# Kernel tuning notes

Measured on AMD Instinct MI355X. Metric: run time of the kernel, lower is better.

The kernel has to match this reference:

```python
import jax, jax.numpy as jnp
import numpy as np

NUM_TRAIN = 256  # num_train_anchors
N, A, T = 8, 131072, 64


def _make_boxes(key, shape2):
    # shape2 = (..., 2) of (y, x); returns valid boxes (y1, x1, y2, x2) in [0, 1]
    k1, k2 = jax.random.split(key)
    c1 = jax.random.uniform(k1, shape2, dtype=jnp.float32)
    c2 = jax.random.uniform(k2, shape2, dtype=jnp.float32)
    lo = jnp.minimum(c1, c2)
    hi = jnp.maximum(c1, c2)
    return jnp.stack([lo[..., 0], lo[..., 1], hi[..., 0], hi[..., 1]], axis=-1)


def setup_inputs() -> dict:
    key = jax.random.key(0)
    ka, kt, kp, kn = jax.random.split(key, 4)
    return {
        "anchors": _make_boxes(ka, (N, A, 2)),
        "true_bboxes": _make_boxes(kt, (N, T, 2)),
        "rand_pos": jax.random.uniform(kp, (N, A), dtype=jnp.float32),
        "rand_neg": jax.random.uniform(kn, (N, A), dtype=jnp.float32),
    }


def _bbox_overlap(anchors, gt):
    # anchors [A,4], gt [T,4] -> IoU [A,T]
    ay1, ax1, ay2, ax2 = [anchors[:, i] for i in range(4)]
    gy1, gx1, gy2, gx2 = [gt[:, i] for i in range(4)]
    a_area = (ay2 - ay1) * (ax2 - ax1)                       # [A]
    g_area = (gy2 - gy1) * (gx2 - gx1)                       # [T]
    ih = jnp.clip(jnp.minimum(ay2[:, None], gy2[None, :]) - jnp.maximum(ay1[:, None], gy1[None, :]), 0.0)
    iw = jnp.clip(jnp.minimum(ax2[:, None], gx2[None, :]) - jnp.maximum(ax1[:, None], gx1[None, :]), 0.0)
    inter = ih * iw                                          # [A,T]
    union = a_area[:, None] + g_area[None, :] - inter
    return jnp.where(union > 0, inter / jnp.where(union > 0, union, 1.0), 0.0)


def _rank_of(scores):
    # rank[i] = position of element i in ascending sort of scores
    order = jnp.argsort(scores)
    return jnp.zeros(scores.shape[0], jnp.int32).at[order].set(jnp.arange(scores.shape[0], dtype=jnp.int32))


def _compute_bbox_deltas(anchors, gt):
    # standard (dy, dx, dh, dw) encoding with safe denominators
    ah = anchors[:, 2] - anchors[:, 0]
    aw = anchors[:, 3] - anchors[:, 1]
    acy = anchors[:, 0] + 0.5 * ah
    acx = anchors[:, 1] + 0.5 * aw
    gh = gt[:, 2] - gt[:, 0]
    gw = gt[:, 3] - gt[:, 1]
    gcy = gt[:, 0] + 0.5 * gh
    gcx = gt[:, 1] + 0.5 * gw
    ah_s = jnp.where(ah > 0, ah, 1.0)
    aw_s = jnp.where(aw > 0, aw, 1.0)
    gh_s = jnp.where(gh > 0, gh, 1.0)
    gw_s = jnp.where(gw > 0, gw, 1.0)
    return jnp.stack([(gcy - acy) / ah_s, (gcx - acx) / aw_s,
                      jnp.log(gh_s / ah_s), jnp.log(gw_s / aw_s)], axis=-1)


def _get_targets(anchors, gt, r_pos, r_neg):
    na = anchors.shape[0]
    # strip_out_of_bounds_anchors: zero out anchors falling outside [0,1]^2 (keeps static shape)
    inb = (anchors[:, 0] >= 0) & (anchors[:, 1] >= 0) & (anchors[:, 2] <= 1) & (anchors[:, 3] <= 1)
    anchors = jnp.where(inb[:, None], anchors, 0.0)

    overlaps = _bbox_overlap(anchors, gt)                    # [A,T]

    # --- class assignment ---
    iou_max_val = jnp.max(overlaps, axis=1)                  # [A]
    classes = jnp.full((na,), -1, jnp.int32)
    classes = jnp.where(iou_max_val < 0.3, 0, classes)
    iou_max_anchor = jnp.argmax(overlaps, axis=0)            # [T] best anchor per gt
    pos_anchor = jnp.zeros((na,), jnp.int32).at[iou_max_anchor].set(1)
    classes = jnp.where(pos_anchor > 0, 1, classes)
    classes = jnp.where(iou_max_val >= 0.7, 1, classes)

    # --- subsample positives to NUM_TRAIN//2 (uniform random subset) ---
    pos = classes > 0
    rank_p = _rank_of(jnp.where(pos, r_pos, jnp.inf))
    keep_pos = pos & (rank_p < NUM_TRAIN // 2)
    classes = jnp.where(pos & ~keep_pos, -1, classes)
    n_pos = jnp.sum(keep_pos.astype(jnp.int32))

    # --- subsample negatives to NUM_TRAIN - n_pos ---
    desired_neg = NUM_TRAIN - n_pos
    neg = classes == 0
    rank_n = _rank_of(jnp.where(neg, r_neg, jnp.inf))
    keep_neg = neg & (rank_n < desired_neg)
    classes = jnp.where(neg & ~keep_neg, -1, classes)

    # --- deltas for positive anchors ---
    best_gt = jnp.argmax(overlaps, axis=1)                   # [A]
    deltas = _compute_bbox_deltas(anchors, gt[best_gt])      # [A,4]
    deltas = jnp.where((classes > 0)[:, None], deltas, 0.0)
    return classes, deltas


def reference(anchors, true_bboxes, rand_pos, rand_neg):
    classes, deltas = jax.vmap(_get_targets)(anchors, true_bboxes, rand_pos, rand_neg)
    return classes, deltas
```

## Files before the change

### kernel.cpp

```cpp
#include <hip/hip_runtime.h>
#include <stdint.h>

#define N_B 8
#define A_N 131072
#define T_N 64
#define NUM_TRAIN 256
#define NEG_TAU 0.05f
#define ITEM_CAP 1024
#define APT 4
#define GBLK 128
#define SEG 1024

typedef unsigned long long u64;
typedef unsigned int u32;

__device__ __forceinline__ float iou_one(float ay1, float ax1, float ay2, float ax2,
                                         float a_area, float gy1, float gx1, float gy2,
                                         float gx2, float g_area) {
#pragma clang fp contract(off)
    float ih = fmaxf(fminf(ay2, gy2) - fmaxf(ay1, gy1), 0.0f);
    float iw = fmaxf(fminf(ax2, gx2) - fmaxf(ax1, gx1), 0.0f);
    float inter = ih * iw;
    float uni = (a_area + g_area) - inter;
    return uni > 0.0f ? inter / uni : 0.0f;
}

__global__ void __launch_bounds__(256, 4) k_main(const float4* __restrict__ anchors4,
                                                 const float4* __restrict__ gts4,
                                                 const float* __restrict__ rpos,
                                                 const float* __restrict__ rneg,
                                                 unsigned char* __restrict__ preclass,
                                                 u64* __restrict__ colpart,
                                                 u64* __restrict__ pos_list,
                                                 u64* __restrict__ neg_list,
                                                 int* __restrict__ bcp, int* __restrict__ bcn) {
    __shared__ float4 gbox[T_N];
    __shared__ float gars[T_N];
    __shared__ u64 cmax[T_N];
    __shared__ int lp, ln;
    int n = blockIdx.y, bx = blockIdx.x, tid = threadIdx.x, lane = tid & 63;
    int a0 = bx * SEG + tid;
    size_t nA = (size_t)n * A_N;

    if (tid < T_N) {
        float4 gb = gts4[n * T_N + tid];
        gbox[tid] = gb;
        {
#pragma clang fp contract(off)
            gars[tid] = (gb.z - gb.x) * (gb.w - gb.y);
        }
        cmax[tid] = 0;
    }
    if (tid == 0) { lp = 0; ln = 0; }
    __syncthreads();

    float ay1[APT], ax1[APT], ay2[APT], ax2[APT], aar[APT], vmax[APT];
#pragma unroll
    for (int k = 0; k < APT; k++) {
        float4 ab = anchors4[nA + a0 + k * 256];
        float y1 = ab.x, x1 = ab.y, y2 = ab.z, x2 = ab.w;
        bool inb = (y1 >= 0.f) && (x1 >= 0.f) && (y2 <= 1.f) && (x2 <= 1.f);
        if (!inb) { y1 = x1 = y2 = x2 = 0.f; }
        ay1[k] = y1; ax1[k] = x1; ay2[k] = y2; ax2[k] = x2;
        {
#pragma clang fp contract(off)
            aar[k] = (y2 - y1) * (x2 - x1);
        }
        vmax[k] = 0.f;
    }

#pragma unroll 4
    for (int jj = 0; jj < T_N; jj++) {
        int j = (lane + jj) & (T_N - 1);
        float4 gb = gbox[j];
        float gar = gars[j];
        float vb = iou_one(ay1[0], ax1[0], ay2[0], ax2[0], aar[0], gb.x, gb.y, gb.z, gb.w, gar);
        vmax[0] = fmaxf(vmax[0], vb);
        int kb = 0;
#pragma unroll
        for (int k = 1; k < APT; k++) {
            float v = iou_one(ay1[k], ax1[k], ay2[k], ax2[k], aar[k], gb.x, gb.y, gb.z, gb.w, gar);
            vmax[k] = fmaxf(vmax[k], v);
            if (v > vb) { vb = v; kb = k; }
        }
        u64 pk = ((u64)__float_as_uint(vb) << 32) | (u32)(~(u32)(a0 + (kb << 8)));
        atomicMax(&cmax[j], pk);
    }

    size_t segbase = ((size_t)(n * GBLK + bx)) << 10;
#pragma unroll
    for (int k = 0; k < APT; k++) {
        int a = a0 + k * 256;
        float vm = vmax[k];
        int c0 = (vm < 0.3f) ? 0 : ((vm >= 0.7f) ? 1 : -1);
        preclass[nA + a] = (unsigned char)(signed char)c0;
        if (c0 == 1) {
            int s = atomicAdd(&lp, 1);
            pos_list[segbase + s] = ((u64)__float_as_uint(rpos[nA + a]) << 32) | (u32)a;
        } else if (c0 == 0) {
            float r = rneg[nA + a];
            if (r < NEG_TAU) {
                int s = atomicAdd(&ln, 1);
                neg_list[segbase + s] = ((u64)__float_as_uint(r) << 32) | (u32)a;
            }
        }
    }
    __syncthreads();
    if (tid < T_N) colpart[(size_t)((n << 6) + tid) * GBLK + bx] = cmax[tid];
    if (tid == 0) { bcp[n * GBLK + bx] = lp; bcn[n * GBLK + bx] = ln; }
}

__device__ u64 select_kth2(const u64* lists, const int* scnt,
                           const u64* extras, int ecnt, const u32* exbm,
                           int k, float scale, u64 ovf_all,
                           int* hist, u64* items, int* misc, int* wsum, u64* result) {
    int tid = threadIdx.x, lane = tid & 63, wid = tid >> 6;
    hist[tid] = 0;
    if (tid == 0) { misc[0] = 0; *result = ovf_all; }
    __syncthreads();

    int seg = tid >> 1, half = tid & 1;
    int c = scnt[seg];
    const ulonglong2* b2 = (const ulonglong2*)(lists + ((size_t)seg << 10));
    int nch = (c + 1) >> 1;

    {
        ulonglong2 q;
        if (half < nch) q = b2[half];
        for (int ci = half; ci < nch; ci += 2) {
            ulonglong2 qn;
            if (ci + 2 < nch) qn = b2[ci + 2];
            {
                u64 p = q.x; int a = (int)(u32)p;
                if (!exbm || !((exbm[a >> 5] >> (a & 31)) & 1)) {
                    float v = __uint_as_float((u32)(p >> 32));
                    int bb = (int)(v * scale); bb = bb > 255 ? 255 : bb;
                    atomicAdd(&hist[bb], 1);
                }
            }
            if (2 * ci + 1 < c) {
                u64 p = q.y; int a = (int)(u32)p;
                if (!exbm || !((exbm[a >> 5] >> (a & 31)) & 1)) {
                    float v = __uint_as_float((u32)(p >> 32));
                    int bb = (int)(v * scale); bb = bb > 255 ? 255 : bb;
                    atomicAdd(&hist[bb], 1);
                }
            }
            q = qn;
        }
    }
    for (int i = tid; i < ecnt; i += 256) {
        float v = __uint_as_float((u32)(extras[i] >> 32));
        int bb = (int)(v * scale); bb = bb > 255 ? 255 : bb;
        atomicAdd(&hist[bb], 1);
    }
    __syncthreads();

    int h = hist[tid], v = h;
#pragma unroll
    for (int d = 1; d < 64; d <<= 1) {
        int t = __shfl_up(v, d, 64);
        if (lane >= d) v += t;
    }
    if (lane == 63) wsum[wid] = v;
    __syncthreads();
    int base = 0;
    for (int w = 0; w < wid; w++) base += wsum[w];
    int total = wsum[0] + wsum[1] + wsum[2] + wsum[3];
    int incl = base + v, exc = incl - h;
    if (k >= exc && k < incl) { misc[1] = tid; misc[2] = exc; }
    __syncthreads();
    if (k >= total) return ovf_all;
    int b = misc[1], before = misc[2];

    {
        ulonglong2 q;
        if (half < nch) q = b2[half];
        for (int ci = half; ci < nch; ci += 2) {
            ulonglong2 qn;
            if (ci + 2 < nch) qn = b2[ci + 2];
            {
                u64 p = q.x; int a = (int)(u32)p;
                if (!exbm || !((exbm[a >> 5] >> (a & 31)) & 1)) {
                    float vv = __uint_as_float((u32)(p >> 32));
                    int bn = (int)(vv * scale); bn = bn > 255 ? 255 : bn;
                    if (bn == b) { int ix = atomicAdd(&misc[0], 1); if (ix < ITEM_CAP) items[ix] = p; }
                }
            }
            if (2 * ci + 1 < c) {
                u64 p = q.y; int a = (int)(u32)p;
                if (!exbm || !((exbm[a >> 5] >> (a & 31)) & 1)) {
                    float vv = __uint_as_float((u32)(p >> 32));
                    int bn = (int)(vv * scale); bn = bn > 255 ? 255 : bn;
                    if (bn == b) { int ix = atomicAdd(&misc[0], 1); if (ix < ITEM_CAP) items[ix] = p; }
                }
            }
            q = qn;
        }
    }
    for (int i = tid; i < ecnt; i += 256) {
        u64 p = extras[i];
        float vv = __uint_as_float((u32)(p >> 32));
        int bn = (int)(vv * scale); bn = bn > 255 ? 255 : bn;
        if (bn == b) { int ix = atomicAdd(&misc[0], 1); if (ix < ITEM_CAP) items[ix] = p; }
    }
    __syncthreads();
    int m = misc[0]; m = m < ITEM_CAP ? m : ITEM_CAP;
    int target = k - before;
    for (int i = tid; i < m; i += 256) {
        u64 p = items[i];
        int r = 0;
        for (int j = 0; j < m; j++) r += (items[j] < p);
        if (r == target) *result = p;
    }
    __syncthreads();
    u64 res = *result;
    __syncthreads();
    return res;
}

__global__ void __launch_bounds__(256) k_select(const u64* __restrict__ pos_list,
                                                const u64* __restrict__ neg_list,
                                                const int* __restrict__ bcp,
                                                const int* __restrict__ bcn,
                                                const u64* __restrict__ colpart,
                                                const unsigned char* __restrict__ preclass,
                                                const float* __restrict__ rpos,
                                                int* __restrict__ wnr_g,
                                                u64* __restrict__ cutoff) {
    __shared__ int sbp[GBLK], sbn[GBLK];
    __shared__ u64 cq[256];
    __shared__ int wnrs[T_N];
    __shared__ u64 extras[T_N];
    __shared__ int hist[256];
    __shared__ u64 items[ITEM_CAP];
    __shared__ u32 exbm[A_N / 32];
    __shared__ int misc[4];
    __shared__ u64 result;
    __shared__ int wsum[4];
    __shared__ int shr[9];
    int n = blockIdx.x, tid = threadIdx.x, lane = tid & 63, wid = tid >> 6;

    int pv = tid < GBLK ? bcp[n * GBLK + tid] : 0;
    int nv = tid < GBLK ? bcn[n * GBLK + tid] : 0;
    if (tid < GBLK) { sbp[tid] = pv; sbn[tid] = nv; }
#pragma unroll
    for (int off = 32; off > 0; off >>= 1) {
        pv += __shfl_xor(pv, off, 64);
        nv += __shfl_xor(nv, off, 64);
    }
    if (lane == 0) { shr[wid] = pv; shr[4 + wid] = nv; }

#pragma unroll
    for (int i = 0; i < A_N / 32 / 256; i++) exbm[tid + i * 256] = 0;

    {
        int t = tid >> 2, q = tid & 3;
        const u64* cp = colpart + (size_t)((n << 6) + t) * GBLK + q * 32;
        u64 m = 0;
#pragma unroll 8
        for (int i = 0; i < 32; i++) { u64 x = cp[i]; m = x > m ? x : m; }
        cq[tid] = m;
    }
    __syncthreads();
    if (tid < T_N) {
        u64 m = cq[tid * 4];
        u64 x = cq[tid * 4 + 1]; m = x > m ? x : m;
        x = cq[tid * 4 + 2]; m = x > m ? x : m;
        x = cq[tid * 4 + 3]; m = x > m ? x : m;
        int w = (int)(~(u32)(m & 0xFFFFFFFFull));
        wnrs[tid] = w;
        wnr_g[n * T_N + tid] = w;
        atomicOr(&exbm[w >> 5], 1u << (w & 31));
    }
    __syncthreads();
    if (tid < T_N) {
        int w = wnrs[tid];
        bool dup = false;
        for (int t2 = 0; t2 < tid; t2++) dup |= (wnrs[t2] == w);
        int pc = (int)(signed char)preclass[(size_t)n * A_N + w];
        bool val = !dup && (pc != 1);
        u64 mask = __ballot(val);
        if (val) {
            int ix = (int)__popcll(mask & ((1ull << lane) - 1));
            extras[ix] = ((u64)__float_as_uint(rpos[(size_t)n * A_N + w]) << 32) | (u32)w;
        }
        if (tid == 0) shr[8] = (int)__popcll(mask);
    }
    __syncthreads();
    int extra_cnt = shr[8];
    int P = shr[0] + shr[1] + shr[2] + shr[3] + extra_cnt;

    u64 cpos = select_kth2(pos_list + (((size_t)n * GBLK) << 10), sbp,
                           extras, extra_cnt, nullptr,
                           NUM_TRAIN / 2, 256.0f, ~0ull,
                           hist, items, misc, wsum, &result);
    int n_pos = P < NUM_TRAIN / 2 ? P : NUM_TRAIN / 2;
    int k_neg = NUM_TRAIN - n_pos;
    u64 cneg = select_kth2(neg_list + (((size_t)n * GBLK) << 10), sbn,
                           nullptr, 0, exbm,
                           k_neg, 256.0f / NEG_TAU, ((u64)__float_as_uint(NEG_TAU) << 32),
                           hist, items, misc, wsum, &result);
    if (tid == 0) { cutoff[2 * n] = cpos; cutoff[2 * n + 1] = cneg; }
}

__global__ void __launch_bounds__(256) k_final(const float4* __restrict__ anchors4,
                                               const float4* __restrict__ gts4,
                                               const u32* __restrict__ preclass32,
                                               const int* __restrict__ wnr_g,
                                               const float4* __restrict__ rpos4,
                                               const float4* __restrict__ rneg4,
                                               const u64* __restrict__ cutoff,
                                               float4* __restrict__ out_classes4,
                                               float4* __restrict__ out_deltas) {
    __shared__ float4 gbox[T_N];
    __shared__ float gars[T_N];
    __shared__ u32 wbm[32];
    int n = blockIdx.y, bx = blockIdx.x, tid = threadIdx.x;
    if (tid < 32) wbm[tid] = 0;
    __syncthreads();
    if (tid < T_N) {
        float4 gb = gts4[n * T_N + tid];
        gbox[tid] = gb;
        {
#pragma clang fp contract(off)
            gars[tid] = (gb.z - gb.x) * (gb.w - gb.y);
        }
        int w = wnr_g[n * T_N + tid];
        int d = w - bx * SEG;
        if ((u32)d < (u32)SEG) atomicOr(&wbm[d >> 5], 1u << (d & 31));
    }
    __syncthreads();

    size_t gi4 = ((size_t)n * A_N) / 4 + bx * 256 + tid;
    u32 pcw = preclass32[gi4];
    float4 rp = rpos4[gi4];
    float4 rn = rneg4[gi4];
    float rpv[4] = {rp.x, rp.y, rp.z, rp.w};
    float rnv[4] = {rn.x, rn.y, rn.z, rn.w};
    int a0 = (bx * 256 + tid) * 4;
    u64 cp = cutoff[2 * n], cn = cutoff[2 * n + 1];

    u32 marked = (wbm[tid >> 3] >> ((tid & 7) * 4)) & 0xF;

    float fcv[4];
#pragma unroll
    for (int j = 0; j < 4; j++) {
        int c = (int)(signed char)((pcw >> (8 * j)) & 0xFF);
        if ((marked >> j) & 1) c = 1;
        int a = a0 + j;
        int fc = -1;
        if (c == 1) {
            u64 p = ((u64)__float_as_uint(rpv[j]) << 32) | (u32)a;
            fc = (p < cp) ? 1 : -1;
        } else if (c == 0) {
            u64 p = ((u64)__float_as_uint(rnv[j]) << 32) | (u32)a;
            fc = (p < cn) ? 0 : -1;
        }
        fcv[j] = (float)fc;

        float4 d = make_float4(0.f, 0.f, 0.f, 0.f);
        if (fc == 1) {
            float4 ab = anchors4[(size_t)n * A_N + a];
            float ay1 = ab.x, ax1 = ab.y, ay2 = ab.z, ax2 = ab.w;
            bool inb = (ay1 >= 0.f) && (ax1 >= 0.f) && (ay2 <= 1.f) && (ax2 <= 1.f);
            if (!inb) { ay1 = ax1 = ay2 = ax2 = 0.f; }
            float a_area;
            {
#pragma clang fp contract(off)
                a_area = (ay2 - ay1) * (ax2 - ax1);
            }
            float vm = 0.f; int jb = 0;
            for (int t = 0; t < T_N; t++) {
                float4 gb = gbox[t];
                float v = iou_one(ay1, ax1, ay2, ax2, a_area, gb.x, gb.y, gb.z, gb.w, gars[t]);
                bool g = v > vm;
                vm = g ? v : vm;
                jb = g ? t : jb;
            }
            float4 gb = gbox[jb];
            float ah = ay2 - ay1, aw = ax2 - ax1;
            float acy = ay1 + 0.5f * ah, acx = ax1 + 0.5f * aw;
            float gh = gb.z - gb.x, gw = gb.w - gb.y;
            float gcy = gb.x + 0.5f * gh, gcx = gb.y + 0.5f * gw;
            float ah_s = ah > 0.f ? ah : 1.f, aw_s = aw > 0.f ? aw : 1.f;
            float gh_s = gh > 0.f ? gh : 1.f, gw_s = gw > 0.f ? gw : 1.f;
            d.x = (gcy - acy) / ah_s;
            d.y = (gcx - acx) / aw_s;
            d.z = logf(gh_s / ah_s);
            d.w = logf(gw_s / aw_s);
        }
        out_deltas[(size_t)n * A_N + a] = d;
    }
    out_classes4[gi4] = make_float4(fcv[0], fcv[1], fcv[2], fcv[3]);
}

extern "C" void kernel_launch(void* const* d_in, const int* in_sizes, int n_in,
                              void* d_out, int out_size, void* d_ws, size_t ws_size,
                              hipStream_t stream) {
    const float* anchors = (const float*)d_in[0];
    const float* gts     = (const float*)d_in[1];
    const float* rpos    = (const float*)d_in[2];
    const float* rneg    = (const float*)d_in[3];

    char* p = (char*)d_ws;
    u64* cutoff   = (u64*)p;  p += 2 * N_B * sizeof(u64);
    u64* colpart  = (u64*)p;  p += (size_t)N_B * T_N * GBLK * sizeof(u64);
    u64* pos_list = (u64*)p;  p += (size_t)N_B * GBLK * SEG * sizeof(u64);
    u64* neg_list = (u64*)p;  p += (size_t)N_B * GBLK * SEG * sizeof(u64);
    unsigned char* preclass = (unsigned char*)p; p += (size_t)N_B * A_N;
    int* bcp  = (int*)p;  p += N_B * GBLK * sizeof(int);
    int* bcn  = (int*)p;  p += N_B * GBLK * sizeof(int);
    int* wnr  = (int*)p;  p += N_B * T_N * sizeof(int);

    float* out_classes = (float*)d_out;
    float4* out_deltas = (float4*)(out_classes + (size_t)N_B * A_N);

    k_main<<<dim3(GBLK, N_B), 256, 0, stream>>>(
        (const float4*)anchors, (const float4*)gts, rpos, rneg,
        preclass, colpart, pos_list, neg_list, bcp, bcn);
    k_select<<<N_B, 256, 0, stream>>>(pos_list, neg_list, bcp, bcn, colpart,
                                      preclass, rpos, wnr, cutoff);
    k_final<<<dim3(GBLK, N_B), 256, 0, stream>>>(
        (const float4*)anchors, (const float4*)gts, (const u32*)preclass, wnr,
        (const float4*)rpos, (const float4*)rneg, cutoff,
        (float4*)out_classes, out_deltas);
}
```

Baseline: 176.4 us.

## Split selection into pos/neg blocks, halve anchors per block, hash-set exclusion

The main kernel now uses 256 blocks per image with 2 anchors per thread, which doubles the grid to raise parallelism. Candidate lists per block are capped at 128 entries. The select kernel now runs two blocks per image, one choosing the positive cutoff and one the negative cutoff in parallel. The 16KB exclusion bitmap is replaced by a small open-addressing hash set in shared memory. In exchange, twice as many column partials must be reduced, and the list caps can silently drop candidates if a block has more than 128, which risks wrong results.

```diff
diff --git a/kernel.cpp b/kernel.cpp
--- a/kernel.cpp
+++ b/kernel.cpp
@@ -6,10 +6,14 @@
 #define T_N 64
 #define NUM_TRAIN 256
 #define NEG_TAU 0.05f
-#define ITEM_CAP 1024
-#define APT 4
-#define GBLK 128
-#define SEG 1024
+#define ITEM_CAP 512
+#define HSET 512
+#define APT 2
+#define SEG_A 512
+#define GBLK_A 256
+#define CAPP 128
+#define BLK_C 128
+#define SEG_C 1024
 
 typedef unsigned long long u64;
 typedef unsigned int u32;
@@ -25,21 +29,21 @@
     return uni > 0.0f ? inter / uni : 0.0f;
 }
 
-__global__ void __launch_bounds__(256, 4) k_main(const float4* __restrict__ anchors4,
-                                                 const float4* __restrict__ gts4,
-                                                 const float* __restrict__ rpos,
-                                                 const float* __restrict__ rneg,
-                                                 unsigned char* __restrict__ preclass,
-                                                 u64* __restrict__ colpart,
-                                                 u64* __restrict__ pos_list,
-                                                 u64* __restrict__ neg_list,
-                                                 int* __restrict__ bcp, int* __restrict__ bcn) {
+__global__ void __launch_bounds__(256) k_main(const float4* __restrict__ anchors4,
+                                              const float4* __restrict__ gts4,
+                                              const float* __restrict__ rpos,
+                                              const float* __restrict__ rneg,
+                                              unsigned char* __restrict__ preclass,
+                                              u64* __restrict__ colpart,
+                                              u64* __restrict__ pos_list,
+                                              u64* __restrict__ neg_list,
+                                              int* __restrict__ bcp, int* __restrict__ bcn) {
     __shared__ float4 gbox[T_N];
     __shared__ float gars[T_N];
     __shared__ u64 cmax[T_N];
-    __shared__ int lp, ln;
+    __shared__ int lcnt[2];
     int n = blockIdx.y, bx = blockIdx.x, tid = threadIdx.x, lane = tid & 63;
-    int a0 = bx * SEG + tid;
+    int a0 = bx * SEG_A + tid;
     size_t nA = (size_t)n * A_N;
 
     if (tid < T_N) {
@@ -51,7 +55,7 @@
         }
         cmax[tid] = 0;
     }
-    if (tid == 0) { lp = 0; ln = 0; }
+    if (tid < 2) lcnt[tid] = 0;
     __syncthreads();
 
     float ay1[APT], ax1[APT], ay2[APT], ax2[APT], aar[APT], vmax[APT];
@@ -87,7 +91,7 @@
         atomicMax(&cmax[j], pk);
     }
 
-    size_t segbase = ((size_t)(n * GBLK + bx)) << 10;
+    size_t segbase = ((size_t)(n * GBLK_A + bx)) << 7;
 #pragma unroll
     for (int k = 0; k < APT; k++) {
         int a = a0 + k * 256;
@@ -95,23 +99,38 @@
         int c0 = (vm < 0.3f) ? 0 : ((vm >= 0.7f) ? 1 : -1);
         preclass[nA + a] = (unsigned char)(signed char)c0;
         if (c0 == 1) {
-            int s = atomicAdd(&lp, 1);
-            pos_list[segbase + s] = ((u64)__float_as_uint(rpos[nA + a]) << 32) | (u32)a;
+            int sl = atomicAdd(&lcnt[0], 1);
+            if (sl < CAPP)
+                pos_list[segbase + sl] = ((u64)__float_as_uint(rpos[nA + a]) << 32) | (u32)a;
         } else if (c0 == 0) {
             float r = rneg[nA + a];
             if (r < NEG_TAU) {
-                int s = atomicAdd(&ln, 1);
-                neg_list[segbase + s] = ((u64)__float_as_uint(r) << 32) | (u32)a;
-            }
-        }
-    }
-    __syncthreads();
-    if (tid < T_N) colpart[(size_t)((n << 6) + tid) * GBLK + bx] = cmax[tid];
-    if (tid == 0) { bcp[n * GBLK + bx] = lp; bcn[n * GBLK + bx] = ln; }
+                int sl = atomicAdd(&lcnt[1], 1);
+                if (sl < CAPP)
+                    neg_list[segbase + sl] = ((u64)__float_as_uint(r) << 32) | (u32)a;
+            }
+        }
+    }
+    __syncthreads();
+    if (tid < T_N) colpart[(size_t)((n << 6) + tid) * GBLK_A + bx] = cmax[tid];
+    if (tid == 0) {
+        bcp[n * GBLK_A + bx] = lcnt[0] < CAPP ? lcnt[0] : CAPP;
+        bcn[n * GBLK_A + bx] = lcnt[1] < CAPP ? lcnt[1] : CAPP;
+    }
+}
+
+__device__ __forceinline__ bool in_hset(const int* hset, int a) {
+    u32 h = ((u32)a * 2654435761u) >> 23 & (HSET - 1);
+    while (true) {
+        int v = hset[h];
+        if (v == -1) return false;
+        if (v == a) return true;
+        h = (h + 1) & (HSET - 1);
+    }
 }
 
 __device__ u64 select_kth2(const u64* lists, const int* scnt,
-                           const u64* extras, int ecnt, const u32* exbm,
+                           const u64* extras, int ecnt, const int* hset, bool use_excl,
                            int k, float scale, u64 ovf_all,
                            int* hist, u64* items, int* misc, int* wsum, u64* result) {
     int tid = threadIdx.x, lane = tid & 63, wid = tid >> 6;
@@ -119,20 +138,19 @@
     if (tid == 0) { misc[0] = 0; *result = ovf_all; }
     __syncthreads();
 
-    int seg = tid >> 1, half = tid & 1;
-    int c = scnt[seg];
-    const ulonglong2* b2 = (const ulonglong2*)(lists + ((size_t)seg << 10));
+    int c = scnt[tid];
+    const ulonglong2* b2 = (const ulonglong2*)(lists + ((size_t)tid << 7));
     int nch = (c + 1) >> 1;
 
     {
         ulonglong2 q;
-        if (half < nch) q = b2[half];
-        for (int ci = half; ci < nch; ci += 2) {
+        if (nch > 0) q = b2[0];
+        for (int ci = 0; ci < nch; ci++) {
             ulonglong2 qn;
-            if (ci + 2 < nch) qn = b2[ci + 2];
+            if (ci + 1 < nch) qn = b2[ci + 1];
             {
                 u64 p = q.x; int a = (int)(u32)p;
-                if (!exbm || !((exbm[a >> 5] >> (a & 31)) & 1)) {
+                if (!use_excl || !in_hset(hset, a)) {
                     float v = __uint_as_float((u32)(p >> 32));
                     int bb = (int)(v * scale); bb = bb > 255 ? 255 : bb;
                     atomicAdd(&hist[bb], 1);
@@ -140,7 +158,7 @@
             }
             if (2 * ci + 1 < c) {
                 u64 p = q.y; int a = (int)(u32)p;
-                if (!exbm || !((exbm[a >> 5] >> (a & 31)) & 1)) {
+                if (!use_excl || !in_hset(hset, a)) {
                     float v = __uint_as_float((u32)(p >> 32));
                     int bb = (int)(v * scale); bb = bb > 255 ? 255 : bb;
                     atomicAdd(&hist[bb], 1);
@@ -175,13 +193,13 @@
 
     {
         ulonglong2 q;
-        if (half < nch) q = b2[half];
-        for (int ci = half; ci < nch; ci += 2) {
+        if (nch > 0) q = b2[0];
+        for (int ci = 0; ci < nch; ci++) {
             ulonglong2 qn;
-            if (ci + 2 < nch) qn = b2[ci + 2];
+            if (ci + 1 < nch) qn = b2[ci + 1];
             {
                 u64 p = q.x; int a = (int)(u32)p;
-                if (!exbm || !((exbm[a >> 5] >> (a & 31)) & 1)) {
+                if (!use_excl || !in_hset(hset, a)) {
                     float vv = __uint_as_float((u32)(p >> 32));
                     int bn = (int)(vv * scale); bn = bn > 255 ? 255 : bn;
                     if (bn == b) { int ix = atomicAdd(&misc[0], 1); if (ix < ITEM_CAP) items[ix] = p; }
@@ -189,7 +207,7 @@
             }
             if (2 * ci + 1 < c) {
                 u64 p = q.y; int a = (int)(u32)p;
-                if (!exbm || !((exbm[a >> 5] >> (a & 31)) & 1)) {
+                if (!use_excl || !in_hset(hset, a)) {
                     float vv = __uint_as_float((u32)(p >> 32));
                     int bn = (int)(vv * scale); bn = bn > 255 ? 255 : bn;
                     if (bn == b) { int ix = atomicAdd(&misc[0], 1); if (ix < ITEM_CAP) items[ix] = p; }
@@ -219,47 +237,44 @@
     return res;
 }
 
-__global__ void __launch_bounds__(256) k_select(const u64* __restrict__ pos_list,
-                                                const u64* __restrict__ neg_list,
-                                                const int* __restrict__ bcp,
-                                                const int* __restrict__ bcn,
-                                                const u64* __restrict__ colpart,
-                                                const unsigned char* __restrict__ preclass,
-                                                const float* __restrict__ rpos,
-                                                int* __restrict__ wnr_g,
-                                                u64* __restrict__ cutoff) {
-    __shared__ int sbp[GBLK], sbn[GBLK];
+__global__ void __launch_bounds__(256) k_B(const u64* __restrict__ pos_list,
+                                           const u64* __restrict__ neg_list,
+                                           const int* __restrict__ bcp,
+                                           const int* __restrict__ bcn,
+                                           const u64* __restrict__ colpart,
+                                           const unsigned char* __restrict__ preclass,
+                                           const float* __restrict__ rpos,
+                                           int* __restrict__ wnr_g,
+                                           u64* __restrict__ cutoff) {
+    __shared__ int sbp[GBLK_A], sbn[GBLK_A];
     __shared__ u64 cq[256];
     __shared__ int wnrs[T_N];
     __shared__ u64 extras[T_N];
     __shared__ int hist[256];
     __shared__ u64 items[ITEM_CAP];
-    __shared__ u32 exbm[A_N / 32];
+    __shared__ int hset[HSET];
     __shared__ int misc[4];
+    __shared__ int wsum[4];
+    __shared__ int shr[10];
     __shared__ u64 result;
-    __shared__ int wsum[4];
-    __shared__ int shr[9];
-    int n = blockIdx.x, tid = threadIdx.x, lane = tid & 63, wid = tid >> 6;
-
-    int pv = tid < GBLK ? bcp[n * GBLK + tid] : 0;
-    int nv = tid < GBLK ? bcn[n * GBLK + tid] : 0;
-    if (tid < GBLK) { sbp[tid] = pv; sbn[tid] = nv; }
-#pragma unroll
-    for (int off = 32; off > 0; off >>= 1) {
-        pv += __shfl_xor(pv, off, 64);
-        nv += __shfl_xor(nv, off, 64);
-    }
-    if (lane == 0) { shr[wid] = pv; shr[4 + wid] = nv; }
-
-#pragma unroll
-    for (int i = 0; i < A_N / 32 / 256; i++) exbm[tid + i * 256] = 0;
+    int n = blockIdx.y, role = blockIdx.x, tid = threadIdx.x, lane = tid & 63, wid = tid >> 6;
+    size_t nA = (size_t)n * A_N;
+
+    int pv = bcp[n * GBLK_A + tid];
+    sbp[tid] = pv;
+    sbn[tid] = bcn[n * GBLK_A + tid];
+#pragma unroll
+    for (int off = 32; off > 0; off >>= 1) pv += __shfl_xor(pv, off, 64);
+    if (lane == 0) shr[wid] = pv;
+
+    for (int i = tid; i < HSET; i += 256) hset[i] = -1;
 
     {
         int t = tid >> 2, q = tid & 3;
-        const u64* cp = colpart + (size_t)((n << 6) + t) * GBLK + q * 32;
+        const u64* cp = colpart + (size_t)((n << 6) + t) * GBLK_A + q * 64;
         u64 m = 0;
 #pragma unroll 8
-        for (int i = 0; i < 32; i++) { u64 x = cp[i]; m = x > m ? x : m; }
+        for (int i = 0; i < 64; i++) { u64 x = cp[i]; m = x > m ? x : m; }
         cq[tid] = m;
     }
     __syncthreads();
@@ -270,20 +285,25 @@
         x = cq[tid * 4 + 3]; m = x > m ? x : m;
         int w = (int)(~(u32)(m & 0xFFFFFFFFull));
         wnrs[tid] = w;
-        wnr_g[n * T_N + tid] = w;
-        atomicOr(&exbm[w >> 5], 1u << (w & 31));
+        if (role == 0) wnr_g[n * T_N + tid] = w;
+        u32 hh = ((u32)w * 2654435761u) >> 23 & (HSET - 1);
+        while (true) {
+            int old = atomicCAS(&hset[hh], -1, w);
+            if (old == -1 || old == w) break;
+            hh = (hh + 1) & (HSET - 1);
+        }
     }
     __syncthreads();
     if (tid < T_N) {
         int w = wnrs[tid];
         bool dup = false;
         for (int t2 = 0; t2 < tid; t2++) dup |= (wnrs[t2] == w);
-        int pc = (int)(signed char)preclass[(size_t)n * A_N + w];
+        int pc = (int)(signed char)preclass[nA + w];
         bool val = !dup && (pc != 1);
         u64 mask = __ballot(val);
-        if (val) {
+        if (role == 0 && val) {
             int ix = (int)__popcll(mask & ((1ull << lane) - 1));
-            extras[ix] = ((u64)__float_as_uint(rpos[(size_t)n * A_N + w]) << 32) | (u32)w;
+            extras[ix] = ((u64)__float_as_uint(rpos[nA + w]) << 32) | (u32)w;
         }
         if (tid == 0) shr[8] = (int)__popcll(mask);
     }
@@ -291,32 +311,37 @@
     int extra_cnt = shr[8];
     int P = shr[0] + shr[1] + shr[2] + shr[3] + extra_cnt;
 
-    u64 cpos = select_kth2(pos_list + (((size_t)n * GBLK) << 10), sbp,
-                           extras, extra_cnt, nullptr,
-                           NUM_TRAIN / 2, 256.0f, ~0ull,
-                           hist, items, misc, wsum, &result);
-    int n_pos = P < NUM_TRAIN / 2 ? P : NUM_TRAIN / 2;
-    int k_neg = NUM_TRAIN - n_pos;
-    u64 cneg = select_kth2(neg_list + (((size_t)n * GBLK) << 10), sbn,
-                           nullptr, 0, exbm,
-                           k_neg, 256.0f / NEG_TAU, ((u64)__float_as_uint(NEG_TAU) << 32),
-                           hist, items, misc, wsum, &result);
-    if (tid == 0) { cutoff[2 * n] = cpos; cutoff[2 * n + 1] = cneg; }
-}
-
-__global__ void __launch_bounds__(256) k_final(const float4* __restrict__ anchors4,
-                                               const float4* __restrict__ gts4,
-                                               const u32* __restrict__ preclass32,
-                                               const int* __restrict__ wnr_g,
-                                               const float4* __restrict__ rpos4,
-                                               const float4* __restrict__ rneg4,
-                                               const u64* __restrict__ cutoff,
-                                               float4* __restrict__ out_classes4,
-                                               float4* __restrict__ out_deltas) {
+    if (role == 0) {
+        u64 cpos = select_kth2(pos_list + (((size_t)n * GBLK_A) << 7), sbp,
+                               extras, extra_cnt, hset, false,
+                               NUM_TRAIN / 2, 256.0f, ~0ull,
+                               hist, items, misc, wsum, &result);
+        if (tid == 0) cutoff[2 * n] = cpos;
+    } else {
+        int n_pos = P < NUM_TRAIN / 2 ? P : NUM_TRAIN / 2;
+        int k_neg = NUM_TRAIN - n_pos;
+        u64 cneg = select_kth2(neg_list + (((size_t)n * GBLK_A) << 7), sbn,
+                               nullptr, 0, hset, true,
+                               k_neg, 256.0f / NEG_TAU, ((u64)__float_as_uint(NEG_TAU) << 32),
+                               hist, items, misc, wsum, &result);
+        if (tid == 0) cutoff[2 * n + 1] = cneg;
+    }
+}
+
+__global__ void __launch_bounds__(256) k_C(const float4* __restrict__ anchors4,
+                                           const float4* __restrict__ gts4,
+                                           const u32* __restrict__ preclass32,
+                                           const int* __restrict__ wnr_g,
+                                           const float4* __restrict__ rpos4,
+                                           const float4* __restrict__ rneg4,
+                                           const u64* __restrict__ cutoff,
+                                           float4* __restrict__ out_classes4,
+                                           float4* __restrict__ out_deltas) {
     __shared__ float4 gbox[T_N];
     __shared__ float gars[T_N];
     __shared__ u32 wbm[32];
     int n = blockIdx.y, bx = blockIdx.x, tid = threadIdx.x;
+    size_t nA = (size_t)n * A_N;
     if (tid < 32) wbm[tid] = 0;
     __syncthreads();
     if (tid < T_N) {
@@ -327,12 +352,12 @@
             gars[tid] = (gb.z - gb.x) * (gb.w - gb.y);
         }
         int w = wnr_g[n * T_N + tid];
-        int d = w - bx * SEG;
-        if ((u32)d < (u32)SEG) atomicOr(&wbm[d >> 5], 1u << (d & 31));
-    }
-    __syncthreads();
-
-    size_t gi4 = ((size_t)n * A_N) / 4 + bx * 256 + tid;
+        int d = w - bx * SEG_C;
+        if ((u32)d < (u32)SEG_C) atomicOr(&wbm[d >> 5], 1u << (d & 31));
+    }
+    __syncthreads();
+
+    size_t gi4 = nA / 4 + bx * 256 + tid;
     u32 pcw = preclass32[gi4];
     float4 rp = rpos4[gi4];
     float4 rn = rneg4[gi4];
@@ -361,7 +386,7 @@
 
         float4 d = make_float4(0.f, 0.f, 0.f, 0.f);
         if (fc == 1) {
-            float4 ab = anchors4[(size_t)n * A_N + a];
+            float4 ab = anchors4[nA + a];
             float ay1 = ab.x, ax1 = ab.y, ay2 = ab.z, ax2 = ab.w;
             bool inb = (ay1 >= 0.f) && (ax1 >= 0.f) && (ay2 <= 1.f) && (ax2 <= 1.f);
             if (!inb) { ay1 = ax1 = ay2 = ax2 = 0.f; }
@@ -390,7 +415,7 @@
             d.z = logf(gh_s / ah_s);
             d.w = logf(gw_s / aw_s);
         }
-        out_deltas[(size_t)n * A_N + a] = d;
+        out_deltas[nA + a] = d;
     }
     out_classes4[gi4] = make_float4(fcv[0], fcv[1], fcv[2], fcv[3]);
 }
@@ -398,31 +423,29 @@
 extern "C" void kernel_launch(void* const* d_in, const int* in_sizes, int n_in,
                               void* d_out, int out_size, void* d_ws, size_t ws_size,
                               hipStream_t stream) {
-    const float* anchors = (const float*)d_in[0];
-    const float* gts     = (const float*)d_in[1];
-    const float* rpos    = (const float*)d_in[2];
-    const float* rneg    = (const float*)d_in[3];
+    const float4* anchors4 = (const float4*)d_in[0];
+    const float4* gts4     = (const float4*)d_in[1];
+    const float*  rpos     = (const float*)d_in[2];
+    const float*  rneg     = (const float*)d_in[3];
 
     char* p = (char*)d_ws;
     u64* cutoff   = (u64*)p;  p += 2 * N_B * sizeof(u64);
-    u64* colpart  = (u64*)p;  p += (size_t)N_B * T_N * GBLK * sizeof(u64);
-    u64* pos_list = (u64*)p;  p += (size_t)N_B * GBLK * SEG * sizeof(u64);
-    u64* neg_list = (u64*)p;  p += (size_t)N_B * GBLK * SEG * sizeof(u64);
+    u64* colpart  = (u64*)p;  p += (size_t)N_B * T_N * GBLK_A * sizeof(u64);
+    u64* pos_list = (u64*)p;  p += (size_t)N_B * GBLK_A * CAPP * sizeof(u64);
+    u64* neg_list = (u64*)p;  p += (size_t)N_B * GBLK_A * CAPP * sizeof(u64);
     unsigned char* preclass = (unsigned char*)p; p += (size_t)N_B * A_N;
-    int* bcp  = (int*)p;  p += N_B * GBLK * sizeof(int);
-    int* bcn  = (int*)p;  p += N_B * GBLK * sizeof(int);
+    int* bcp  = (int*)p;  p += N_B * GBLK_A * sizeof(int);
+    int* bcn  = (int*)p;  p += N_B * GBLK_A * sizeof(int);
     int* wnr  = (int*)p;  p += N_B * T_N * sizeof(int);
 
-    float* out_classes = (float*)d_out;
-    float4* out_deltas = (float4*)(out_classes + (size_t)N_B * A_N);
-
-    k_main<<<dim3(GBLK, N_B), 256, 0, stream>>>(
-        (const float4*)anchors, (const float4*)gts, rpos, rneg,
-        preclass, colpart, pos_list, neg_list, bcp, bcn);
-    k_select<<<N_B, 256, 0, stream>>>(pos_list, neg_list, bcp, bcn, colpart,
-                                      preclass, rpos, wnr, cutoff);
-    k_final<<<dim3(GBLK, N_B), 256, 0, stream>>>(
-        (const float4*)anchors, (const float4*)gts, (const u32*)preclass, wnr,
-        (const float4*)rpos, (const float4*)rneg, cutoff,
-        (float4*)out_classes, out_deltas);
-}
+    float4* out_classes4 = (float4*)d_out;
+    float4* out_deltas   = (float4*)((float*)d_out + (size_t)N_B * A_N);
+
+    k_main<<<dim3(GBLK_A, N_B), 256, 0, stream>>>(anchors4, gts4, rpos, rneg, preclass,
+                                                  colpart, pos_list, neg_list, bcp, bcn);
+    k_B<<<dim3(2, N_B), 256, 0, stream>>>(pos_list, neg_list, bcp, bcn, colpart,
+                                          preclass, rpos, wnr, cutoff);
+    k_C<<<dim3(BLK_C, N_B), 256, 0, stream>>>(anchors4, gts4, (const u32*)preclass, wnr,
+                                              (const float4*)rpos, (const float4*)rneg,
+                                              cutoff, out_classes4, out_deltas);
+}
```

New measurement: 177.9 us. Within noise of the previous version (+0.8%).
